# Performance work log

Measured on AMD Instinct MI355X. Metric: run time of the kernel, lower is better.

## Reference

```python
import jax, jax.numpy as jnp
import numpy as np

N_CLASSES = 9
N_GROUPS = 2


def setup_inputs() -> dict:
    key = jax.random.key(0)
    k1, k2 = jax.random.split(key)
    N = 16_777_216  # number of samples
    preds = jax.random.randint(k1, (N,), 0, N_CLASSES, dtype=jnp.int32)
    attrs = jax.random.randint(k2, (N,), 0, N_GROUPS, dtype=jnp.int32)
    return {"preds": preds, "attrs": attrs}


def reference(preds, attrs):
    # Fused histogram: flatten (class, group) -> single bin id in [0, 18)
    flat = preds * N_GROUPS + attrs  # [N]
    counts = jax.ops.segment_sum(
        jnp.ones_like(flat, dtype=jnp.float32), flat,
        num_segments=N_CLASSES * N_GROUPS,
    ).reshape(N_CLASSES, N_GROUPS)  # [9, 2] histogram

    n_attr_1 = jnp.sum(attrs != 0).astype(jnp.float32)
    n_attr_0 = jnp.float32(attrs.shape[0]) - n_attr_1

    diff = counts[:, 0] / n_attr_0 - counts[:, 1] / n_attr_1  # [9]
    return jnp.sum(diff * diff)
```

## Files before the change

kernel.cpp:

```cpp
#include <hip/hip_runtime.h>


#define N_CLASSES 9
#define N_GROUPS 2
#define NBINS (N_CLASSES * N_GROUPS)
#define BDIM 512
#define ITEMS 4
#define NITER 4
#define SPAN (BDIM * ITEMS)
#define BLOCKSPAN (SPAN * NITER)

typedef int vint4 __attribute__((ext_vector_type(4)));

__global__ __launch_bounds__(BDIM, 4) void spd_hist_kernel(
    const int* __restrict__ preds,
    const int* __restrict__ attrs,
    unsigned int* __restrict__ partials,
    int n4, int n)
{
    __shared__ unsigned int lh0[N_CLASSES];
    __shared__ unsigned int lh1[N_CLASSES];
    if (threadIdx.x < N_CLASSES) { lh0[threadIdx.x] = 0u; lh1[threadIdx.x] = 0u; }
    __syncthreads();

    unsigned int cnt[N_CLASSES];
    #pragma unroll
    for (int p = 0; p < N_CLASSES; ++p) cnt[p] = 0u;

    const vint4* __restrict__ p4 = (const vint4*)preds;
    const vint4* __restrict__ a4 = (const vint4*)attrs;

    for (int S = blockIdx.x * BLOCKSPAN; S < n4; S += gridDim.x * BLOCKSPAN) {
        const int s = S + (int)threadIdx.x;
        unsigned long long accT = 0ull, acc1 = 0ull;

        if (S + BLOCKSPAN <= n4) {
            vint4 aP0, aP1, aP2, aP3, aA0, aA1, aA2, aA3;
            vint4 bP0, bP1, bP2, bP3, bA0, bA1, bA2, bA3;

            #define LDBUF(B, base) \
                B##P0 = p4[(base)];            B##A0 = a4[(base)]; \
                B##P1 = p4[(base) + BDIM];     B##A1 = a4[(base) + BDIM]; \
                B##P2 = p4[(base) + 2*BDIM];   B##A2 = a4[(base) + 2*BDIM]; \
                B##P3 = p4[(base) + 3*BDIM];   B##A3 = a4[(base) + 3*BDIM];

            #define PIN(B) asm volatile("" : \
                "+v"(B##P0), "+v"(B##P1), "+v"(B##P2), "+v"(B##P3), \
                "+v"(B##A0), "+v"(B##A1), "+v"(B##A2), "+v"(B##A3) :: "memory");

            #define CONS1(P, A) { \
                { unsigned long long inc = 1ull << (7 * P.x); accT += inc; acc1 += (A.x == 0) ? 0ull : inc; } \
                { unsigned long long inc = 1ull << (7 * P.y); accT += inc; acc1 += (A.y == 0) ? 0ull : inc; } \
                { unsigned long long inc = 1ull << (7 * P.z); accT += inc; acc1 += (A.z == 0) ? 0ull : inc; } \
                { unsigned long long inc = 1ull << (7 * P.w); accT += inc; acc1 += (A.w == 0) ? 0ull : inc; } \
            }
            #define CONSBUF(B) \
                CONS1(B##P0, B##A0) CONS1(B##P1, B##A1) \
                CONS1(B##P2, B##A2) CONS1(B##P3, B##A3)

            LDBUF(a, s)
            LDBUF(b, s + SPAN)
            PIN(a) CONSBUF(a)
            LDBUF(a, s + 2 * SPAN)
            PIN(b) CONSBUF(b)
            LDBUF(b, s + 3 * SPAN)
            PIN(a) CONSBUF(a)
            PIN(b) CONSBUF(b)

            #undef LDBUF
            #undef PIN
            #undef CONS1
            #undef CONSBUF
        } else {
            for (int m = 0; m < NITER * ITEMS; ++m) {
                const int idx = s + m * BDIM;
                if (idx < n4) {
                    vint4 pp = p4[idx];
                    vint4 aa = a4[idx];
                    {
                        unsigned long long inc = 1ull << (7 * pp.x);
                        accT += inc; acc1 += (aa.x == 0) ? 0ull : inc;
                    }
                    {
                        unsigned long long inc = 1ull << (7 * pp.y);
                        accT += inc; acc1 += (aa.y == 0) ? 0ull : inc;
                    }
                    {
                        unsigned long long inc = 1ull << (7 * pp.z);
                        accT += inc; acc1 += (aa.z == 0) ? 0ull : inc;
                    }
                    {
                        unsigned long long inc = 1ull << (7 * pp.w);
                        accT += inc; acc1 += (aa.w == 0) ? 0ull : inc;
                    }
                }
            }
        }

        #pragma unroll
        for (int p = 0; p < N_CLASSES; ++p) {
            unsigned int ct = (unsigned int)(accT >> (7 * p)) & 127u;
            unsigned int c1 = (unsigned int)(acc1 >> (7 * p)) & 127u;
            cnt[p] += (ct - c1) | (c1 << 16);
        }
    }

    if (blockIdx.x == 0) {
        for (int t = n4 * 4 + (int)threadIdx.x; t < n; t += BDIM)
            cnt[preds[t]] += (attrs[t] == 0) ? 1u : 0x10000u;
    }

    #pragma unroll
    for (int m = 1; m < 64; m <<= 1) {
        #pragma unroll
        for (int p = 0; p < N_CLASSES; ++p)
            cnt[p] += __shfl_xor(cnt[p], m, 64);
    }

    if ((threadIdx.x & 63) == 0) {
        #pragma unroll
        for (int p = 0; p < N_CLASSES; ++p) {
            atomicAdd(&lh0[p], cnt[p] & 0xFFFFu);
            atomicAdd(&lh1[p], cnt[p] >> 16);
        }
    }
    __syncthreads();

    if (threadIdx.x < NBINS) {
        int c = threadIdx.x >> 1;
        unsigned int v = (threadIdx.x & 1) ? lh1[c] : lh0[c];
        partials[blockIdx.x * NBINS + threadIdx.x] = v;
    }
}

__global__ __launch_bounds__(1024) void spd_finalize_kernel(
    const unsigned int* __restrict__ partials,
    float* __restrict__ out, int nblocks, double n_total)
{
    __shared__ double counts[NBINS];
    const int tid = threadIdx.x;

    if (tid < NBINS * 32) {
        const int bin = tid >> 5;
        const int j = tid & 31;
        unsigned int s = 0u;
        #pragma unroll 8
        for (int b = j; b < nblocks; b += 32)
            s += partials[b * NBINS + bin];
        #pragma unroll
        for (int m = 1; m < 32; m <<= 1)
            s += __shfl_xor(s, m, 32);
        if (j == 0) counts[bin] = (double)s;
    }
    __syncthreads();

    if (tid == 0) {
        double n1 = 0.0;
        #pragma unroll
        for (int c = 0; c < N_CLASSES; ++c)
            n1 += counts[c * N_GROUPS + 1];
        double n0 = n_total - n1;
        double acc = 0.0;
        #pragma unroll
        for (int c = 0; c < N_CLASSES; ++c) {
            double d = counts[c * N_GROUPS] / n0 - counts[c * N_GROUPS + 1] / n1;
            acc += d * d;
        }
        out[0] = (float)acc;
    }
}

extern "C" void kernel_launch(void* const* d_in, const int* in_sizes, int n_in,
                              void* d_out, int out_size, void* d_ws, size_t ws_size,
                              hipStream_t stream)
{
    const int* preds = (const int*)d_in[0];
    const int* attrs = (const int*)d_in[1];
    const int n = in_sizes[0];

    unsigned int* partials = (unsigned int*)d_ws;

    const int n4 = n / 4;
    int grid = (n4 + BLOCKSPAN - 1) / BLOCKSPAN;
    if (grid > 1024) grid = 1024;
    int max_grid = (int)(ws_size / (NBINS * sizeof(unsigned int)));
    if (grid > max_grid) grid = max_grid;
    if (grid < 1) grid = 1;

    spd_hist_kernel<<<grid, BDIM, 0, stream>>>(preds, attrs, partials, n4, n);
    spd_finalize_kernel<<<1, 1024, 0, stream>>>(partials, (float*)d_out, grid, (double)n);
}
```

Baseline: 150.2 us.

## Issue all per-thread loads via inline asm with staged vmcnt waits

Replaces the two-buffer software pipeline (4 items × 4 iterations) with a single stage of 8 items per thread. All 16 dwordx4 loads are issued up front through inline assembly, then consumed in order behind progressively relaxed s_waitcnt vmcnt barriers. It also lowers the occupancy hint to 2 blocks per CU and raises the grid cap to 2048. The goal is more memory-level parallelism per thread and less wait overhead. The cost is higher register pressure, and the hand-written waitcnt counts could break if the compiler inserts other memory operations.

```diff
diff --git a/kernel.cpp b/kernel.cpp
--- a/kernel.cpp
+++ b/kernel.cpp
@@ -5,14 +5,12 @@
 #define N_GROUPS 2
 #define NBINS (N_CLASSES * N_GROUPS)
 #define BDIM 512
-#define ITEMS 4
-#define NITER 4
-#define SPAN (BDIM * ITEMS)
-#define BLOCKSPAN (SPAN * NITER)
+#define ITEMS 8
+#define BLOCKSPAN (BDIM * ITEMS)
 
 typedef int vint4 __attribute__((ext_vector_type(4)));
 
-__global__ __launch_bounds__(BDIM, 4) void spd_hist_kernel(
+__global__ __launch_bounds__(BDIM, 2) void spd_hist_kernel(
     const int* __restrict__ preds,
     const int* __restrict__ attrs,
     unsigned int* __restrict__ partials,
@@ -31,22 +29,46 @@
     const vint4* __restrict__ a4 = (const vint4*)attrs;
 
     for (int S = blockIdx.x * BLOCKSPAN; S < n4; S += gridDim.x * BLOCKSPAN) {
-        const int s = S + (int)threadIdx.x;
         unsigned long long accT = 0ull, acc1 = 0ull;
 
         if (S + BLOCKSPAN <= n4) {
-            vint4 aP0, aP1, aP2, aP3, aA0, aA1, aA2, aA3;
-            vint4 bP0, bP1, bP2, bP3, bA0, bA1, bA2, bA3;
-
-            #define LDBUF(B, base) \
-                B##P0 = p4[(base)];            B##A0 = a4[(base)]; \
-                B##P1 = p4[(base) + BDIM];     B##A1 = a4[(base) + BDIM]; \
-                B##P2 = p4[(base) + 2*BDIM];   B##A2 = a4[(base) + 2*BDIM]; \
-                B##P3 = p4[(base) + 3*BDIM];   B##A3 = a4[(base) + 3*BDIM];
-
-            #define PIN(B) asm volatile("" : \
-                "+v"(B##P0), "+v"(B##P1), "+v"(B##P2), "+v"(B##P3), \
-                "+v"(B##A0), "+v"(B##A1), "+v"(B##A2), "+v"(B##A3) :: "memory");
+            unsigned int off0 = ((unsigned int)(S + (int)threadIdx.x)) * 16u;
+            unsigned int o0 = off0;
+            unsigned int o1 = off0 + 1u * BDIM * 16u;
+            unsigned int o2 = off0 + 2u * BDIM * 16u;
+            unsigned int o3 = off0 + 3u * BDIM * 16u;
+            unsigned int o4 = off0 + 4u * BDIM * 16u;
+            unsigned int o5 = off0 + 5u * BDIM * 16u;
+            unsigned int o6 = off0 + 6u * BDIM * 16u;
+            unsigned int o7 = off0 + 7u * BDIM * 16u;
+
+            vint4 P0, P1, P2, P3, P4, P5, P6, P7;
+            vint4 A0, A1, A2, A3, A4, A5, A6, A7;
+
+            asm volatile(
+                "global_load_dwordx4 %0, %16, %24\n\t"
+                "global_load_dwordx4 %8, %16, %25\n\t"
+                "global_load_dwordx4 %1, %17, %24\n\t"
+                "global_load_dwordx4 %9, %17, %25\n\t"
+                "global_load_dwordx4 %2, %18, %24\n\t"
+                "global_load_dwordx4 %10, %18, %25\n\t"
+                "global_load_dwordx4 %3, %19, %24\n\t"
+                "global_load_dwordx4 %11, %19, %25\n\t"
+                "global_load_dwordx4 %4, %20, %24\n\t"
+                "global_load_dwordx4 %12, %20, %25\n\t"
+                "global_load_dwordx4 %5, %21, %24\n\t"
+                "global_load_dwordx4 %13, %21, %25\n\t"
+                "global_load_dwordx4 %6, %22, %24\n\t"
+                "global_load_dwordx4 %14, %22, %25\n\t"
+                "global_load_dwordx4 %7, %23, %24\n\t"
+                "global_load_dwordx4 %15, %23, %25"
+                : "=&v"(P0), "=&v"(P1), "=&v"(P2), "=&v"(P3),
+                  "=&v"(P4), "=&v"(P5), "=&v"(P6), "=&v"(P7),
+                  "=&v"(A0), "=&v"(A1), "=&v"(A2), "=&v"(A3),
+                  "=&v"(A4), "=&v"(A5), "=&v"(A6), "=&v"(A7)
+                : "v"(o0), "v"(o1), "v"(o2), "v"(o3),
+                  "v"(o4), "v"(o5), "v"(o6), "v"(o7),
+                  "s"(preds), "s"(attrs));
 
             #define CONS1(P, A) { \
                 { unsigned long long inc = 1ull << (7 * P.x); accT += inc; acc1 += (A.x == 0) ? 0ull : inc; } \
@@ -54,25 +76,18 @@
                 { unsigned long long inc = 1ull << (7 * P.z); accT += inc; acc1 += (A.z == 0) ? 0ull : inc; } \
                 { unsigned long long inc = 1ull << (7 * P.w); accT += inc; acc1 += (A.w == 0) ? 0ull : inc; } \
             }
-            #define CONSBUF(B) \
-                CONS1(B##P0, B##A0) CONS1(B##P1, B##A1) \
-                CONS1(B##P2, B##A2) CONS1(B##P3, B##A3)
-
-            LDBUF(a, s)
-            LDBUF(b, s + SPAN)
-            PIN(a) CONSBUF(a)
-            LDBUF(a, s + 2 * SPAN)
-            PIN(b) CONSBUF(b)
-            LDBUF(b, s + 3 * SPAN)
-            PIN(a) CONSBUF(a)
-            PIN(b) CONSBUF(b)
-
-            #undef LDBUF
-            #undef PIN
+            #define STAGE(k, VM) \
+                asm volatile("s_waitcnt vmcnt(" #VM ")"); \
+                __builtin_amdgcn_sched_barrier(0); \
+                CONS1(P##k, A##k)
+
+            STAGE(0, 14) STAGE(1, 12) STAGE(2, 10) STAGE(3, 8)
+            STAGE(4, 6)  STAGE(5, 4)  STAGE(6, 2)  STAGE(7, 0)
+            #undef STAGE
             #undef CONS1
-            #undef CONSBUF
         } else {
-            for (int m = 0; m < NITER * ITEMS; ++m) {
+            const int s = S + (int)threadIdx.x;
+            for (int m = 0; m < ITEMS; ++m) {
                 const int idx = s + m * BDIM;
                 if (idx < n4) {
                     vint4 pp = p4[idx];
@@ -182,7 +197,7 @@
 
     const int n4 = n / 4;
     int grid = (n4 + BLOCKSPAN - 1) / BLOCKSPAN;
-    if (grid > 1024) grid = 1024;
+    if (grid > 2048) grid = 2048;
     int max_grid = (int)(ws_size / (NBINS * sizeof(unsigned int)));
     if (grid > max_grid) grid = max_grid;
     if (grid < 1) grid = 1;
```

Result: no change. 149.6 us (-0.4%).

## Stream inputs through LDS with async global_load_lds quad-buffered pipeline

Applied to the files above, without the earlier changes.

Replaces the register double-buffered loads with a 4-stage pipeline that uses global_load_lds to copy the preds and attrs tiles directly into shared memory. Each wave waits with explicit vmcnt and reads its slice back with ds_read_b128. The grid is also fixed at 512 persistent blocks with occupancy 2, and the packed 7-bit counters are flushed every 4 tiles. The aim is to keep more memory requests in flight and cut register pressure on this bandwidth-bound histogram, at the cost of extra LDS traffic and hand-written waitcnt sequences that could be fragile.

```diff
diff --git a/kernel.cpp b/kernel.cpp
--- a/kernel.cpp
+++ b/kernel.cpp
@@ -5,19 +5,20 @@
 #define N_GROUPS 2
 #define NBINS (N_CLASSES * N_GROUPS)
 #define BDIM 512
-#define ITEMS 4
-#define NITER 4
-#define SPAN (BDIM * ITEMS)
-#define BLOCKSPAN (SPAN * NITER)
+#define NBUF 4
 
 typedef int vint4 __attribute__((ext_vector_type(4)));
-
-__global__ __launch_bounds__(BDIM, 4) void spd_hist_kernel(
+typedef __attribute__((address_space(1))) const void as1_cvoid;
+typedef __attribute__((address_space(3))) void as3_void;
+
+__global__ __launch_bounds__(BDIM, 2) void spd_hist_kernel(
     const int* __restrict__ preds,
     const int* __restrict__ attrs,
     unsigned int* __restrict__ partials,
     int n4, int n)
 {
+    __shared__ vint4 sp[NBUF][BDIM];
+    __shared__ vint4 sa[NBUF][BDIM];
     __shared__ unsigned int lh0[N_CLASSES];
     __shared__ unsigned int lh1[N_CLASSES];
     if (threadIdx.x < N_CLASSES) { lh0[threadIdx.x] = 0u; lh1[threadIdx.x] = 0u; }
@@ -30,80 +31,95 @@
     const vint4* __restrict__ p4 = (const vint4*)preds;
     const vint4* __restrict__ a4 = (const vint4*)attrs;
 
-    for (int S = blockIdx.x * BLOCKSPAN; S < n4; S += gridDim.x * BLOCKSPAN) {
-        const int s = S + (int)threadIdx.x;
-        unsigned long long accT = 0ull, acc1 = 0ull;
-
-        if (S + BLOCKSPAN <= n4) {
-            vint4 aP0, aP1, aP2, aP3, aA0, aA1, aA2, aA3;
-            vint4 bP0, bP1, bP2, bP3, bA0, bA1, bA2, bA3;
-
-            #define LDBUF(B, base) \
-                B##P0 = p4[(base)];            B##A0 = a4[(base)]; \
-                B##P1 = p4[(base) + BDIM];     B##A1 = a4[(base) + BDIM]; \
-                B##P2 = p4[(base) + 2*BDIM];   B##A2 = a4[(base) + 2*BDIM]; \
-                B##P3 = p4[(base) + 3*BDIM];   B##A3 = a4[(base) + 3*BDIM];
-
-            #define PIN(B) asm volatile("" : \
-                "+v"(B##P0), "+v"(B##P1), "+v"(B##P2), "+v"(B##P3), \
-                "+v"(B##A0), "+v"(B##A1), "+v"(B##A2), "+v"(B##A3) :: "memory");
-
-            #define CONS1(P, A) { \
-                { unsigned long long inc = 1ull << (7 * P.x); accT += inc; acc1 += (A.x == 0) ? 0ull : inc; } \
-                { unsigned long long inc = 1ull << (7 * P.y); accT += inc; acc1 += (A.y == 0) ? 0ull : inc; } \
-                { unsigned long long inc = 1ull << (7 * P.z); accT += inc; acc1 += (A.z == 0) ? 0ull : inc; } \
-                { unsigned long long inc = 1ull << (7 * P.w); accT += inc; acc1 += (A.w == 0) ? 0ull : inc; } \
-            }
-            #define CONSBUF(B) \
-                CONS1(B##P0, B##A0) CONS1(B##P1, B##A1) \
-                CONS1(B##P2, B##A2) CONS1(B##P3, B##A3)
-
-            LDBUF(a, s)
-            LDBUF(b, s + SPAN)
-            PIN(a) CONSBUF(a)
-            LDBUF(a, s + 2 * SPAN)
-            PIN(b) CONSBUF(b)
-            LDBUF(b, s + 3 * SPAN)
-            PIN(a) CONSBUF(a)
-            PIN(b) CONSBUF(b)
-
-            #undef LDBUF
-            #undef PIN
-            #undef CONS1
-            #undef CONSBUF
-        } else {
-            for (int m = 0; m < NITER * ITEMS; ++m) {
-                const int idx = s + m * BDIM;
-                if (idx < n4) {
-                    vint4 pp = p4[idx];
-                    vint4 aa = a4[idx];
-                    {
-                        unsigned long long inc = 1ull << (7 * pp.x);
-                        accT += inc; acc1 += (aa.x == 0) ? 0ull : inc;
-                    }
-                    {
-                        unsigned long long inc = 1ull << (7 * pp.y);
-                        accT += inc; acc1 += (aa.y == 0) ? 0ull : inc;
-                    }
-                    {
-                        unsigned long long inc = 1ull << (7 * pp.z);
-                        accT += inc; acc1 += (aa.z == 0) ? 0ull : inc;
-                    }
-                    {
-                        unsigned long long inc = 1ull << (7 * pp.w);
-                        accT += inc; acc1 += (aa.w == 0) ? 0ull : inc;
-                    }
-                }
-            }
-        }
-
-        #pragma unroll
-        for (int p = 0; p < N_CLASSES; ++p) {
-            unsigned int ct = (unsigned int)(accT >> (7 * p)) & 127u;
-            unsigned int c1 = (unsigned int)(acc1 >> (7 * p)) & 127u;
-            cnt[p] += (ct - c1) | (c1 << 16);
-        }
-    }
+    const int wave = (int)threadIdx.x >> 6;
+    const int lane = (int)threadIdx.x & 63;
+
+    const int F = n4 / BDIM;
+    const int K = ((int)blockIdx.x < F)
+                ? ((F - 1 - (int)blockIdx.x) / (int)gridDim.x + 1) : 0;
+
+    unsigned long long accT = 0ull, acc1 = 0ull;
+
+    #define STAGE(b, j) { \
+        size_t g_ = ((size_t)blockIdx.x + (size_t)(j) * gridDim.x) * BDIM + (size_t)(wave * 64 + lane); \
+        __builtin_amdgcn_global_load_lds((as1_cvoid*)(p4 + g_), (as3_void*)&sp[b][wave * 64], 16, 0, 0); \
+        __builtin_amdgcn_global_load_lds((as1_cvoid*)(a4 + g_), (as3_void*)&sa[b][wave * 64], 16, 0, 0); \
+    }
+
+    #define CONS1(P, A) { \
+        { unsigned long long inc = 1ull << (7 * P.x); accT += inc; acc1 += (A.x == 0) ? 0ull : inc; } \
+        { unsigned long long inc = 1ull << (7 * P.y); accT += inc; acc1 += (A.y == 0) ? 0ull : inc; } \
+        { unsigned long long inc = 1ull << (7 * P.z); accT += inc; acc1 += (A.z == 0) ? 0ull : inc; } \
+        { unsigned long long inc = 1ull << (7 * P.w); accT += inc; acc1 += (A.w == 0) ? 0ull : inc; } \
+    }
+
+    #define FLUSH { \
+        _Pragma("unroll") \
+        for (int p = 0; p < N_CLASSES; ++p) { \
+            unsigned int ct = (unsigned int)(accT >> (7 * p)) & 127u; \
+            unsigned int c1 = (unsigned int)(acc1 >> (7 * p)) & 127u; \
+            cnt[p] += (ct - c1) | (c1 << 16); \
+        } \
+        accT = 0ull; acc1 = 0ull; \
+    }
+
+    #define PIPE(b, VM, DO_STAGE, jn) { \
+        asm volatile("s_waitcnt vmcnt(" #VM ")" ::: "memory"); \
+        __builtin_amdgcn_sched_barrier(0); \
+        unsigned po_ = (unsigned)(uintptr_t)(as3_void*)&sp[b][threadIdx.x]; \
+        unsigned ao_ = (unsigned)(uintptr_t)(as3_void*)&sa[b][threadIdx.x]; \
+        vint4 pp_, aa_; \
+        asm volatile("ds_read_b128 %0, %2\n\t" \
+                     "ds_read_b128 %1, %3\n\t" \
+                     "s_waitcnt lgkmcnt(0)" \
+            : "=&v"(pp_), "=&v"(aa_) : "v"(po_), "v"(ao_) : "memory"); \
+        __builtin_amdgcn_sched_barrier(0); \
+        if (DO_STAGE) STAGE(b, jn) \
+        CONS1(pp_, aa_) \
+    }
+
+    if (K >= NBUF) {
+        STAGE(0, 0) STAGE(1, 1) STAGE(2, 2) STAGE(3, 3)
+        int base = 0;
+        for (; base + 2 * NBUF <= K; base += NBUF) {
+            PIPE(0, 6, 1, base + 4)
+            PIPE(1, 6, 1, base + 5)
+            PIPE(2, 6, 1, base + 6)
+            PIPE(3, 6, 1, base + 7)
+            FLUSH
+        }
+        PIPE(0, 6, 0, 0)
+        PIPE(1, 4, 0, 0)
+        PIPE(2, 2, 0, 0)
+        PIPE(3, 0, 0, 0)
+        for (int j = base + 4; j < K; ++j) {
+            size_t g = ((size_t)blockIdx.x + (size_t)j * gridDim.x) * BDIM + threadIdx.x;
+            vint4 pp = p4[g], aa = a4[g];
+            CONS1(pp, aa)
+        }
+        FLUSH
+    } else {
+        for (int j = 0; j < K; ++j) {
+            size_t g = ((size_t)blockIdx.x + (size_t)j * gridDim.x) * BDIM + threadIdx.x;
+            vint4 pp = p4[g], aa = a4[g];
+            CONS1(pp, aa)
+        }
+        FLUSH
+    }
+
+    if ((n4 % BDIM) && (int)blockIdx.x == (F % (int)gridDim.x)) {
+        size_t g = (size_t)F * BDIM + threadIdx.x;
+        if (g < (size_t)n4) {
+            vint4 pp = p4[g], aa = a4[g];
+            CONS1(pp, aa)
+        }
+        FLUSH
+    }
+
+    #undef PIPE
+    #undef FLUSH
+    #undef CONS1
+    #undef STAGE
 
     if (blockIdx.x == 0) {
         for (int t = n4 * 4 + (int)threadIdx.x; t < n; t += BDIM)
@@ -181,8 +197,9 @@
     unsigned int* partials = (unsigned int*)d_ws;
 
     const int n4 = n / 4;
-    int grid = (n4 + BLOCKSPAN - 1) / BLOCKSPAN;
-    if (grid > 1024) grid = 1024;
+    const int F = n4 / BDIM;
+    int grid = 512;
+    if (grid > F) grid = (F > 0) ? F : 1;
     int max_grid = (int)(ws_size / (NBINS * sizeof(unsigned int)));
     if (grid > max_grid) grid = max_grid;
     if (grid < 1) grid = 1;
```

Measured after the change: 150.5 us. Within noise of the previous version (+0.2%).
